# Performance work log

Hardware: AMD Instinct MI355X
Metric: run time of the kernel (lower is better)

Reference implementation:

```python
import jax, jax.numpy as jnp
import numpy as np

THRESH = 64.0        # titans.surprise_threshold
NOISE_SCALE = 1e-6   # tie-breaking noise scale in _update_memory


def setup_inputs() -> dict:
    key = jax.random.key(0)
    ks = jax.random.split(key, 8)
    B, S, H, M = 2, 2048, 1024, 8192
    return {
        "hidden_states": jax.random.normal(ks[0], (B, S, H), dtype=jnp.float32),
        "memory_buffer": jax.random.normal(ks[1], (M, H), dtype=jnp.float32),
        "importance_scores": jax.random.uniform(ks[2], (M,), dtype=jnp.float32),
        "Wq": jax.random.normal(ks[3], (H, H), dtype=jnp.float32) * 0.02,
        "bq": jnp.zeros((H,), dtype=jnp.float32),
        "Wk": jax.random.normal(ks[4], (H, H), dtype=jnp.float32) * 0.02,
        "bk": jnp.zeros((H,), dtype=jnp.float32),
        "noise": jax.random.normal(ks[5], (M,), dtype=jnp.float32),
    }


def reference(hidden_states, memory_buffer, importance_scores, Wq, bq, Wk, bk, noise):
    B, S, H = hidden_states.shape
    M = memory_buffer.shape[0]

    # ---- surprise (gradient_norm method) ----
    # proxy_loss = sum((h - 0)^2)  =>  d loss / d h = 2h  =>  surprise = 2*||h||_2
    cands = hidden_states.reshape(-1, H)                      # [B*S, H]
    surprise = 2.0 * jnp.linalg.norm(cands, axis=-1)          # [B*S]

    # ---- _update_memory (torch.no_grad) ----
    # mask below-threshold candidates out, then take the (at most memory_size)
    # most surprising candidates in descending order (== argsort descending +
    # slice in the torch code; -inf entries sort last and are marked invalid).
    K = min(cands.shape[0], M)
    masked = jnp.where(surprise > THRESH, surprise, -jnp.inf)
    top_s, top_i = jax.lax.top_k(masked, K)                   # descending surprise
    valid = top_s > THRESH                                    # true only for real candidates

    # least-important memory slots (topk largest=False with tie-break noise)
    _, least_idx = jax.lax.top_k(-(importance_scores + noise * NOISE_SCALE), K)

    # scatter-write: i-th most surprising candidate -> i-th least important slot.
    # invalid lanes write to index M which is dropped (out of range).
    write_idx = jnp.where(valid, least_idx, M)                # [K]
    states_w = jax.lax.stop_gradient(cands[top_i])            # update path is no_grad
    scores_w = jax.lax.stop_gradient(jnp.where(valid, top_s, 0.0))
    new_buffer = memory_buffer.at[write_idx].set(states_w, mode="drop")   # [M, H]
    new_importance = importance_scores.at[write_idx].set(scores_w, mode="drop")
    del new_importance  # bookkeeping state; does not affect retrieved output

    # ---- query (cross-attention over memory) ----
    q = hidden_states @ Wq.T + bq                             # [B, S, H]
    mk = new_buffer @ Wk.T + bk                               # [M, H]
    scores = jnp.einsum("bsh,mh->bsm", q, mk) * (H ** -0.5)
    attn = jax.nn.softmax(scores, axis=-1)                    # [B, S, M]
    retrieved = jnp.einsum("bsm,mh->bsh", attn, new_buffer)   # [B, S, H]
    return retrieved
```

## Files before the change

### kernel.cpp

```cpp
#include <hip/hip_runtime.h>
#include <hip/hip_bf16.h>
#include <math.h>
#include <stdint.h>

typedef __attribute__((ext_vector_type(4))) float floatx4;
typedef __attribute__((ext_vector_type(8))) short shortx8;
typedef __attribute__((ext_vector_type(8))) unsigned short ushortx8;
typedef __attribute__((ext_vector_type(4))) unsigned short ushortx4;

#define BS_CAND 4096
#define HDIM    1024
#define MSLOTS  8192
#define THRESH  64.0f
#define PV_SPLIT 4
#define PS_COLS 128

__device__ __forceinline__ unsigned short f2b_bits(float f) {
    __hip_bfloat16 b = __float2bfloat16(f);
    return *(unsigned short*)&b;
}
__device__ __forceinline__ float b2f_bits(unsigned short u) {
    return __uint_as_float(((unsigned)u) << 16);
}

__device__ __forceinline__ float blockReduceSum(float x) {
    __shared__ float red[4];
    #pragma unroll
    for (int o = 32; o > 0; o >>= 1) x += __shfl_down(x, o, 64);
    int lane = threadIdx.x & 63, w = threadIdx.x >> 6;
    if (lane == 0) red[w] = x;
    __syncthreads();
    float s = red[0] + red[1] + red[2] + red[3];
    __syncthreads();
    return s;
}

__global__ __launch_bounds__(256) void pre_k(const float* __restrict__ h,
                                             float* __restrict__ sur,
                                             __hip_bfloat16* __restrict__ Hbf,
                                             const float* __restrict__ imp,
                                             const float* __restrict__ noi,
                                             float* __restrict__ keys,
                                             int* __restrict__ row_src,
                                             const float* __restrict__ Wq,
                                             __hip_bfloat16* __restrict__ Wqbf,
                                             const float* __restrict__ Wk,
                                             __hip_bfloat16* __restrict__ Wkbf) {
    int b = blockIdx.x;
    if (b < BS_CAND) {
        float4 v = ((const float4*)(h + (size_t)b * HDIM))[threadIdx.x];
        ushortx4 o;
        o.x = f2b_bits(v.x); o.y = f2b_bits(v.y);
        o.z = f2b_bits(v.z); o.w = f2b_bits(v.w);
        ((ushortx4*)(Hbf + (size_t)b * HDIM))[threadIdx.x] = o;
        float s = v.x * v.x + v.y * v.y + v.z * v.z + v.w * v.w;
        float tot = blockReduceSum(s);
        if (threadIdx.x == 0) sur[b] = 2.0f * sqrtf(tot);
    } else if (b < BS_CAND + MSLOTS / 256) {
        int i = (b - BS_CAND) * 256 + threadIdx.x;
        keys[i] = imp[i] + noi[i] * 1e-6f;
        row_src[i] = -1;
    } else {
        int w = b - (BS_CAND + MSLOTS / 256);
        const float* in = (w < 1024) ? Wq : Wk;
        __hip_bfloat16* out = (w < 1024) ? Wqbf : Wkbf;
        int j = (w & 1023) * 256 + threadIdx.x;
        float4 v = ((const float4*)in)[j];
        ushortx4 o;
        o.x = f2b_bits(v.x); o.y = f2b_bits(v.y);
        o.z = f2b_bits(v.z); o.w = f2b_bits(v.w);
        ((ushortx4*)out)[j] = o;
    }
}

__global__ __launch_bounds__(256) void ranks_k(const float* __restrict__ sur,
                                               int* __restrict__ cand_ord,
                                               const float* __restrict__ keys,
                                               int* __restrict__ slot_ord) {
    int b = blockIdx.x;
    if (b < BS_CAND) {
        float ki = sur[b];
        float cnt = 0.f;
        for (int j = threadIdx.x; j < BS_CAND; j += 256) {
            float kj = sur[j];
            cnt += ((kj > ki) || (kj == ki && j < b)) ? 1.f : 0.f;
        }
        float r = blockReduceSum(cnt);
        if (threadIdx.x == 0) cand_ord[(int)r] = b;
    } else {
        int i = b - BS_CAND;
        float ki = keys[i];
        float cnt = 0.f;
        for (int j = threadIdx.x; j < MSLOTS; j += 256) {
            float kj = keys[j];
            cnt += ((kj < ki) || (kj == ki && j < i)) ? 1.f : 0.f;
        }
        float r = blockReduceSum(cnt);
        if (threadIdx.x == 0) slot_ord[(int)r] = i;
    }
}

__global__ __launch_bounds__(256) void scatter_k(const int* __restrict__ cand_order,
                                                 const int* __restrict__ slot_order,
                                                 const float* __restrict__ sur,
                                                 int* __restrict__ row_src) {
    int i = blockIdx.x * 256 + threadIdx.x;
    int c = cand_order[i];
    if (sur[c] > THRESH) row_src[slot_order[i]] = c;
}

__global__ __launch_bounds__(256) void build_b_k(const float* __restrict__ mem,
                                                 const float* __restrict__ hid,
                                                 const int* __restrict__ src,
                                                 __hip_bfloat16* __restrict__ B) {
    int m = blockIdx.x;
    int s = src[m];
    const float4* r = (const float4*)((s < 0) ? (mem + (size_t)m * HDIM)
                                              : (hid + (size_t)s * HDIM));
    float4 v = r[threadIdx.x];
    ushortx4 o;
    o.x = f2b_bits(v.x); o.y = f2b_bits(v.y);
    o.z = f2b_bits(v.z); o.w = f2b_bits(v.w);
    ((ushortx4*)(B + (size_t)m * HDIM))[threadIdx.x] = o;
}

__global__ __launch_bounds__(256) void transpose_k(const __hip_bfloat16* __restrict__ in,
                                                   __hip_bfloat16* __restrict__ out,
                                                   int R, int C) {
    __shared__ __hip_bfloat16 t[64][65];
    int cb = blockIdx.x * 64, rb = blockIdx.y * 64;
    int tx = threadIdx.x & 63, ty = threadIdx.x >> 6;
    #pragma unroll
    for (int k = 0; k < 16; k++) {
        int r = ty * 16 + k;
        t[r][tx] = in[(size_t)(rb + r) * C + cb + tx];
    }
    __syncthreads();
    #pragma unroll
    for (int k = 0; k < 16; k++) {
        int c = ty * 16 + k;
        out[(size_t)(cb + c) * R + rb + tx] = t[tx][c];
    }
}

__device__ __forceinline__ void load_lds16(const __hip_bfloat16* g, __hip_bfloat16* l) {
    __builtin_amdgcn_global_load_lds(
        (const __attribute__((address_space(1))) void*)g,
        (__attribute__((address_space(3))) void*)l, 16, 0, 0);
}

template <int EPI, int SWAP>
__global__ __launch_bounds__(256) void gemm_bt(const __hip_bfloat16* __restrict__ A,
                                               const __hip_bfloat16* __restrict__ Bt,
                                               const __hip_bfloat16* __restrict__ Bt2,
                                               __hip_bfloat16* __restrict__ outH,
                                               const float* __restrict__ bias,
                                               const float* __restrict__ bias2,
                                               float* __restrict__ ps,
                                               int rows0b,
                                               int M, int N, int K, int ksplit,
                                               float scale) {
    __shared__ alignas(16) __hip_bfloat16 Asm[2][128 * 32];
    __shared__ alignas(16) __hip_bfloat16 Bsm[2][128 * 32];
    const int tid = threadIdx.x;
    const int wave = tid >> 6, lane = tid & 63;
    const int bm = SWAP ? blockIdx.x : blockIdx.y;
    const int bn = SWAP ? blockIdx.y : blockIdx.x;
    const int kb = blockIdx.z * ksplit, ke = kb + ksplit;
    const int wr = (wave >> 1) * 64, wc = (wave & 1) * 64;
    const int lm = lane & 15, lq = lane >> 4;

    const __hip_bfloat16* BtSel = (EPI == 1 && bm >= rows0b) ? Bt2 : Bt;
    const float* biasSel = (EPI == 1 && bm >= rows0b) ? bias2 : bias;

    floatx4 acc[4][4];
    #pragma unroll
    for (int i = 0; i < 4; i++)
        #pragma unroll
        for (int j = 0; j < 4; j++) acc[i][j] = {0.f, 0.f, 0.f, 0.f};

    const __hip_bfloat16* Abase = A + (size_t)bm * 128 * K;
    const __hip_bfloat16* Bbase = BtSel + (size_t)bn * 128 * K;

    for (int k0 = kb; k0 < ke; k0 += 64) {
        #pragma unroll
        for (int t = 0; t < 4; t++) {
            int g = wave * 4 + t;
            int p = g >> 3;
            int pcb = (g & 7) << 6;
            int pc = pcb + lane;
            int row = pc >> 2, cc = pc & 3;
            load_lds16(Abase + (size_t)row * K + k0 + p * 32 + cc * 8,
                       &Asm[p][pcb * 8]);
        }
        #pragma unroll
        for (int t = 0; t < 4; t++) {
            int g = wave * 4 + t;
            int p = g >> 3;
            int pcb = (g & 7) << 6;
            int pc = pcb + lane;
            int row = pc >> 2, cc = pc & 3;
            load_lds16(Bbase + (size_t)row * K + k0 + p * 32 + cc * 8,
                       &Bsm[p][pcb * 8]);
        }
        __syncthreads();
        #pragma unroll
        for (int ks = 0; ks < 2; ks++) {
            shortx8 af[4], bfr[4];
            #pragma unroll
            for (int i = 0; i < 4; i++)
                af[i] = *(const shortx8*)(&Asm[ks][(wr + i * 16 + lm) * 32 + lq * 8]);
            #pragma unroll
            for (int j = 0; j < 4; j++)
                bfr[j] = *(const shortx8*)(&Bsm[ks][(wc + j * 16 + lm) * 32 + lq * 8]);
            #pragma unroll
            for (int i = 0; i < 4; i++)
                #pragma unroll
                for (int j = 0; j < 4; j++)
                    acc[i][j] = __builtin_amdgcn_mfma_f32_16x16x32_bf16(af[i], bfr[j],
                                                                        acc[i][j], 0, 0, 0);
        }
        __syncthreads();
    }

    if (EPI == 2) {
        #pragma unroll
        for (int i = 0; i < 4; i++) {
            int grow0 = bm * 128 + wr + i * 16 + lq * 4;
            #pragma unroll
            for (int r = 0; r < 4; r++) {
                float rs = 0.f;
                #pragma unroll
                for (int j = 0; j < 4; j++) {
                    int gcol = bn * 128 + wc + j * 16 + lm;
                    float e = __expf(acc[i][j][r] * scale);
                    unsigned short eb = f2b_bits(e);
                    ((unsigned short*)outH)[(size_t)(grow0 + r) * N + gcol] = eb;
                    rs += b2f_bits(eb);
                }
                rs += __shfl_xor(rs, 1, 64);
                rs += __shfl_xor(rs, 2, 64);
                rs += __shfl_xor(rs, 4, 64);
                rs += __shfl_xor(rs, 8, 64);
                if (lm == 0)
                    ps[(size_t)(grow0 + r) * PS_COLS + bn * 2 + (wave & 1)] = rs;
            }
        }
    } else {
        __hip_bfloat16* outHz = outH + ((EPI == 4) ? (size_t)blockIdx.z * M * N : 0);
        #pragma unroll
        for (int i = 0; i < 4; i++) {
            int grow0 = bm * 128 + wr + i * 16 + lq * 4;
            #pragma unroll
            for (int j = 0; j < 4; j++) {
                int gcol = bn * 128 + wc + j * 16 + lm;
                #pragma unroll
                for (int r = 0; r < 4; r++) {
                    float v = acc[i][j][r];
                    size_t idx = (size_t)(grow0 + r) * N + gcol;
                    if (EPI == 1) outHz[idx] = __float2bfloat16(v + biasSel[gcol]);
                    else          outHz[idx] = __float2bfloat16(v * scale);
                }
            }
        }
    }
}

__global__ __launch_bounds__(256) void reduce4_k(const ushortx4* __restrict__ part,
                                                 const float* __restrict__ ps,
                                                 float4* __restrict__ out) {
    int row = blockIdx.x;
    float s = 0.f;
    if (threadIdx.x < PS_COLS) s = ps[(size_t)row * PS_COLS + threadIdx.x];
    float tot = blockReduceSum(s);
    float inv = 1.f / tot;
    size_t base = (size_t)row * (HDIM / 4) + threadIdx.x;
    const size_t stride = (size_t)BS_CAND * (HDIM / 4);
    float4 o = {0.f, 0.f, 0.f, 0.f};
    #pragma unroll
    for (int z = 0; z < PV_SPLIT; z++) {
        ushortx4 p = part[base + (size_t)z * stride];
        o.x += b2f_bits(p.x); o.y += b2f_bits(p.y);
        o.z += b2f_bits(p.z); o.w += b2f_bits(p.w);
    }
    o.x *= inv; o.y *= inv; o.z *= inv; o.w *= inv;
    out[(size_t)row * (HDIM / 4) + threadIdx.x] = o;
}

extern "C" void kernel_launch(void* const* d_in, const int* in_sizes, int n_in,
                              void* d_out, int out_size, void* d_ws, size_t ws_size,
                              hipStream_t stream) {
    const float* hidden = (const float*)d_in[0];
    const float* membuf = (const float*)d_in[1];
    const float* imp    = (const float*)d_in[2];
    const float* Wq     = (const float*)d_in[3];
    const float* bq     = (const float*)d_in[4];
    const float* Wk     = (const float*)d_in[5];
    const float* bk     = (const float*)d_in[6];
    const float* noise  = (const float*)d_in[7];

    char* ws = (char*)d_ws;
    size_t off = 0;
    auto alloc = [&](size_t bytes) -> void* {
        void* p = ws + off;
        off += (bytes + 255) & ~(size_t)255;
        return p;
    };
    float*          surprise = (float*)alloc(BS_CAND * 4);
    float*          skeys    = (float*)alloc(MSLOTS * 4);
    float*          ps       = (float*)alloc((size_t)BS_CAND * PS_COLS * 4);
    int*            cand_ord = (int*)alloc(BS_CAND * 4);
    int*            slot_ord = (int*)alloc(MSLOTS * 4);
    int*            row_src  = (int*)alloc(MSLOTS * 4);
    __hip_bfloat16* Wqbf = (__hip_bfloat16*)alloc((size_t)HDIM * HDIM * 2);
    __hip_bfloat16* Wkbf = (__hip_bfloat16*)alloc((size_t)HDIM * HDIM * 2);
    __hip_bfloat16* BbfT = (__hip_bfloat16*)alloc((size_t)HDIM * MSLOTS * 2);
    size_t s_base = off;
    __hip_bfloat16* Sbf = (__hip_bfloat16*)(ws + s_base);
    __hip_bfloat16* Hbf = (__hip_bfloat16*)(ws + s_base);
    __hip_bfloat16* Bbf = (__hip_bfloat16*)(ws + s_base + (size_t)BS_CAND * HDIM * 2);
    off = s_base + ((size_t)BS_CAND * MSLOTS * 2 + 255) & ~(size_t)255;
    size_t t_base = off;
    __hip_bfloat16* qbf  = (__hip_bfloat16*)alloc((size_t)BS_CAND * HDIM * 2);
    __hip_bfloat16* mkbf = (__hip_bfloat16*)alloc((size_t)MSLOTS * HDIM * 2);
    __hip_bfloat16* part = (__hip_bfloat16*)(ws + t_base);

    pre_k<<<BS_CAND + MSLOTS / 256 + 2048, 256, 0, stream>>>(
        hidden, surprise, Hbf, imp, noise, skeys, row_src, Wq, Wqbf, Wk, Wkbf);
    ranks_k<<<BS_CAND + MSLOTS, 256, 0, stream>>>(surprise, cand_ord, skeys, slot_ord);
    scatter_k<<<BS_CAND / 256, 256, 0, stream>>>(cand_ord, slot_ord, surprise, row_src);
    build_b_k<<<MSLOTS, 256, 0, stream>>>(membuf, hidden, row_src, Bbf);
    transpose_k<<<dim3(HDIM / 64, MSLOTS / 64), 256, 0, stream>>>(Bbf, BbfT, MSLOTS, HDIM);
    gemm_bt<1, 0><<<dim3(HDIM / 128, (BS_CAND + MSLOTS) / 128), 256, 0, stream>>>(
        Hbf, Wqbf, Wkbf, qbf, bq, bk, nullptr, BS_CAND / 128,
        BS_CAND + MSLOTS, HDIM, HDIM, HDIM, 1.f);
    gemm_bt<2, 0><<<dim3(MSLOTS / 128, BS_CAND / 128), 256, 0, stream>>>(
        qbf, mkbf, nullptr, Sbf, nullptr, nullptr, ps, 1 << 30,
        BS_CAND, MSLOTS, HDIM, HDIM, 0.03125f);
    gemm_bt<4, 1><<<dim3(BS_CAND / 128, HDIM / 128, PV_SPLIT), 256, 0, stream>>>(
        Sbf, BbfT, nullptr, part, nullptr, nullptr, nullptr, 1 << 30,
        BS_CAND, HDIM, MSLOTS, MSLOTS / PV_SPLIT, 1.f);
    reduce4_k<<<BS_CAND, 256, 0, stream>>>((const ushortx4*)part, ps, (float4*)d_out);
}
```

Measured before the change: 364.1 us.

## Rewrite bf16 GEMM with 256x256 tiles, swizzled LDS and double-buffered pipeline

Replaces the 128x128, 4-wave GEMM with a 256x256 tile computed by 8 waves, each holding an 8x4 grid of MFMA accumulators. It stages 128-wide K slices into 128 KB of XOR-swizzled dynamic LDS with double buffering. Global-to-LDS loads are interleaved with MFMA quadrants using explicit barriers, vmcnt/lgkmcnt waits and s_setprio. The aim is more data reuse per LDS load, fewer bank conflicts and overlap of memory traffic with compute. In exchange, grids get smaller (the projection GEMM has only 192 blocks) and only one block fits per CU, so occupancy and the hand-written wait counts are a risk.

```diff
diff --git a/kernel.cpp b/kernel.cpp
--- a/kernel.cpp
+++ b/kernel.cpp
@@ -5,7 +5,6 @@
 
 typedef __attribute__((ext_vector_type(4))) float floatx4;
 typedef __attribute__((ext_vector_type(8))) short shortx8;
-typedef __attribute__((ext_vector_type(8))) unsigned short ushortx8;
 typedef __attribute__((ext_vector_type(4))) unsigned short ushortx4;
 
 #define BS_CAND 4096
@@ -150,89 +149,165 @@
 }
 
 template <int EPI, int SWAP>
-__global__ __launch_bounds__(256) void gemm_bt(const __hip_bfloat16* __restrict__ A,
-                                               const __hip_bfloat16* __restrict__ Bt,
-                                               const __hip_bfloat16* __restrict__ Bt2,
-                                               __hip_bfloat16* __restrict__ outH,
-                                               const float* __restrict__ bias,
-                                               const float* __restrict__ bias2,
-                                               float* __restrict__ ps,
-                                               int rows0b,
-                                               int M, int N, int K, int ksplit,
-                                               float scale) {
-    __shared__ alignas(16) __hip_bfloat16 Asm[2][128 * 32];
-    __shared__ alignas(16) __hip_bfloat16 Bsm[2][128 * 32];
+__global__ __launch_bounds__(512, 2) void gemm_bt(const __hip_bfloat16* __restrict__ A,
+                                                  const __hip_bfloat16* __restrict__ Bt,
+                                                  const __hip_bfloat16* __restrict__ Bt2,
+                                                  __hip_bfloat16* __restrict__ outH,
+                                                  const float* __restrict__ bias,
+                                                  const float* __restrict__ bias2,
+                                                  float* __restrict__ ps,
+                                                  int rows0b,
+                                                  int M, int N, int K, int ksplit,
+                                                  float scale) {
+    extern __shared__ char lds[];
     const int tid = threadIdx.x;
     const int wave = tid >> 6, lane = tid & 63;
+    const int lm = lane & 15, lq = lane >> 4;
+    const int wm = wave >> 2, wn = wave & 3;
     const int bm = SWAP ? blockIdx.x : blockIdx.y;
     const int bn = SWAP ? blockIdx.y : blockIdx.x;
-    const int kb = blockIdx.z * ksplit, ke = kb + ksplit;
-    const int wr = (wave >> 1) * 64, wc = (wave & 1) * 64;
-    const int lm = lane & 15, lq = lane >> 4;
+    const int kb = blockIdx.z * ksplit;
+    const int niters = ksplit >> 7;
 
     const __hip_bfloat16* BtSel = (EPI == 1 && bm >= rows0b) ? Bt2 : Bt;
     const float* biasSel = (EPI == 1 && bm >= rows0b) ? bias2 : bias;
 
-    floatx4 acc[4][4];
-    #pragma unroll
-    for (int i = 0; i < 4; i++)
+    const int l8 = lane >> 3;
+    const int colsrc = ((((lane & 7) << 4) ^ (l8 << 4)) >> 1);
+    const __hip_bfloat16* Abase = A + (size_t)bm * 256 * K;
+    const __hip_bfloat16* Bbase = BtSel + (size_t)bn * 256 * K;
+    const __hip_bfloat16* srcA[2][2];
+    const __hip_bfloat16* srcB[2][2];
+    #pragma unroll
+    for (int h = 0; h < 2; h++)
+        #pragma unroll
+        for (int t = 0; t < 2; t++) {
+            int row = t * 128 + h * 64 + wave * 8 + l8;
+            srcA[h][t] = Abase + (size_t)row * K + colsrc;
+            srcB[h][t] = Bbase + (size_t)row * K + colsrc;
+        }
+
+    const int cxor = (lq << 4) ^ ((lm & 7) << 4);
+    const int a_b0 = (wm * 64 + lm) * 128 + cxor;
+    const int a_b1 = a_b0 ^ 64;
+    const int b_b0 = (wn * 32 + lm) * 128 + cxor;
+    const int b_b1 = b_b0 ^ 64;
+
+    floatx4 acc[8][4];
+    #pragma unroll
+    for (int i = 0; i < 8; i++)
         #pragma unroll
         for (int j = 0; j < 4; j++) acc[i][j] = {0.f, 0.f, 0.f, 0.f};
 
-    const __hip_bfloat16* Abase = A + (size_t)bm * 128 * K;
-    const __hip_bfloat16* Bbase = BtSel + (size_t)bn * 128 * K;
-
-    for (int k0 = kb; k0 < ke; k0 += 64) {
-        #pragma unroll
-        for (int t = 0; t < 4; t++) {
-            int g = wave * 4 + t;
-            int p = g >> 3;
-            int pcb = (g & 7) << 6;
-            int pc = pcb + lane;
-            int row = pc >> 2, cc = pc & 3;
-            load_lds16(Abase + (size_t)row * K + k0 + p * 32 + cc * 8,
-                       &Asm[p][pcb * 8]);
-        }
-        #pragma unroll
-        for (int t = 0; t < 4; t++) {
-            int g = wave * 4 + t;
-            int p = g >> 3;
-            int pcb = (g & 7) << 6;
-            int pc = pcb + lane;
-            int row = pc >> 2, cc = pc & 3;
-            load_lds16(Bbase + (size_t)row * K + k0 + p * 32 + cc * 8,
-                       &Bsm[p][pcb * 8]);
-        }
-        __syncthreads();
-        #pragma unroll
-        for (int ks = 0; ks < 2; ks++) {
-            shortx8 af[4], bfr[4];
-            #pragma unroll
-            for (int i = 0; i < 4; i++)
-                af[i] = *(const shortx8*)(&Asm[ks][(wr + i * 16 + lm) * 32 + lq * 8]);
-            #pragma unroll
-            for (int j = 0; j < 4; j++)
-                bfr[j] = *(const shortx8*)(&Bsm[ks][(wc + j * 16 + lm) * 32 + lq * 8]);
-            #pragma unroll
-            for (int i = 0; i < 4; i++)
-                #pragma unroll
-                for (int j = 0; j < 4; j++)
-                    acc[i][j] = __builtin_amdgcn_mfma_f32_16x16x32_bf16(af[i], bfr[j],
-                                                                        acc[i][j], 0, 0, 0);
-        }
-        __syncthreads();
-    }
+    shortx8 af[4][2], bf[2][2];
+
+#define LDSV(off) (*(const shortx8*)(lds + (off)))
+#define READ_A(g, bo) do {                                                  \
+    const int ab_ = (bo) + (g) * 16384;                                     \
+    af[0][0] = LDSV(ab_ + a_b0);        af[0][1] = LDSV(ab_ + a_b1);        \
+    af[1][0] = LDSV(ab_ + a_b0 + 2048); af[1][1] = LDSV(ab_ + a_b1 + 2048); \
+    af[2][0] = LDSV(ab_ + a_b0 + 4096); af[2][1] = LDSV(ab_ + a_b1 + 4096); \
+    af[3][0] = LDSV(ab_ + a_b0 + 6144); af[3][1] = LDSV(ab_ + a_b1 + 6144); \
+} while (0)
+#define READ_B(g, bo) do {                                                  \
+    const int bb_ = (bo) + 32768 + (g) * 16384;                             \
+    bf[0][0] = LDSV(bb_ + b_b0);        bf[0][1] = LDSV(bb_ + b_b1);        \
+    bf[1][0] = LDSV(bb_ + b_b0 + 2048); bf[1][1] = LDSV(bb_ + b_b1 + 2048); \
+} while (0)
+#define STAGE(xs, h, buf, kofs) do {                                        \
+    char* d_ = lds + (buf) * 65536 + (xs) * 32768 + (h) * 16384 + wave * 1024; \
+    load_lds16(((xs) ? srcB : srcA)[h][0] + (kofs), (__hip_bfloat16*)d_);   \
+    load_lds16(((xs) ? srcB : srcA)[h][1] + (kofs), (__hip_bfloat16*)(d_ + 8192)); \
+} while (0)
+#define MFQ(mh, nh) do {                                                    \
+    __builtin_amdgcn_s_setprio(1);                                          \
+    _Pragma("unroll")                                                       \
+    for (int ii_ = 0; ii_ < 4; ii_++)                                       \
+        _Pragma("unroll")                                                   \
+        for (int jj_ = 0; jj_ < 2; jj_++) {                                 \
+            acc[(mh)*4+ii_][(nh)*2+jj_] = __builtin_amdgcn_mfma_f32_16x16x32_bf16( \
+                af[ii_][0], bf[jj_][0], acc[(mh)*4+ii_][(nh)*2+jj_], 0, 0, 0); \
+            acc[(mh)*4+ii_][(nh)*2+jj_] = __builtin_amdgcn_mfma_f32_16x16x32_bf16( \
+                af[ii_][1], bf[jj_][1], acc[(mh)*4+ii_][(nh)*2+jj_], 0, 0, 0); \
+        }                                                                   \
+    __builtin_amdgcn_s_setprio(0);                                          \
+} while (0)
+#define BAR() __builtin_amdgcn_s_barrier()
+#define LGKM0() asm volatile("s_waitcnt lgkmcnt(0)" ::: "memory")
+#define VMC6() asm volatile("s_waitcnt vmcnt(6)" ::: "memory")
+#define VMC0() asm volatile("s_waitcnt vmcnt(0)" ::: "memory")
+
+    STAGE(0, 0, 0, kb);
+    STAGE(1, 1, 0, kb);
+    STAGE(0, 1, 0, kb);
+    STAGE(1, 0, 0, kb);
+    STAGE(0, 0, 1, kb + 64);
+    STAGE(1, 1, 1, kb + 64);
+    STAGE(0, 1, 1, kb + 64);
+    VMC6();
+    BAR();
+
+#define ITER(E, kcur, knext) do {                                           \
+                                         \
+    READ_A(0, 0); READ_B(0, 0); STAGE(1, 0, 1, (kcur) + 64);                \
+    BAR(); LGKM0(); MFQ(0, 0); BAR();                                       \
+                                                                   \
+    READ_B(1, 0); if (E) STAGE(0, 0, 0, (knext));                           \
+    BAR(); LGKM0(); MFQ(0, 1); BAR();                                       \
+                                                                   \
+    READ_A(1, 0); if (E) STAGE(1, 1, 0, (knext));                           \
+    BAR(); LGKM0(); MFQ(1, 1); BAR();                                       \
+                                                                   \
+    READ_B(0, 0);                                                           \
+    if (E) { STAGE(0, 1, 0, (knext)); VMC6(); } else { VMC0(); }            \
+    BAR(); LGKM0(); MFQ(1, 0); BAR();                                       \
+                                         \
+    READ_A(0, 65536); READ_B(0, 65536); if (E) STAGE(1, 0, 0, (knext));     \
+    BAR(); LGKM0(); MFQ(0, 0); BAR();                                       \
+                                                                   \
+    READ_B(1, 65536); if (E) STAGE(0, 0, 1, (knext) + 64);                  \
+    BAR(); LGKM0(); MFQ(0, 1); BAR();                                       \
+                                                                   \
+    READ_A(1, 65536); if (E) STAGE(1, 1, 1, (knext) + 64);                  \
+    BAR(); LGKM0(); MFQ(1, 1); BAR();                                       \
+                                                                   \
+    READ_B(0, 65536); if (E) { STAGE(0, 1, 1, (knext) + 64); VMC6(); }      \
+    BAR(); LGKM0(); MFQ(1, 0); BAR();                                       \
+} while (0)
+
+    int it = 0;
+    #pragma unroll 1
+    for (; it < niters - 1; ++it) {
+        const int kc = kb + it * 128;
+        ITER(1, kc, kc + 128);
+    }
+    {
+        const int kc = kb + it * 128;
+        ITER(0, kc, 0);
+    }
+
+#undef ITER
+#undef LDSV
+#undef READ_A
+#undef READ_B
+#undef STAGE
+#undef MFQ
+#undef BAR
+#undef LGKM0
+#undef VMC6
+#undef VMC0
 
     if (EPI == 2) {
         #pragma unroll
-        for (int i = 0; i < 4; i++) {
-            int grow0 = bm * 128 + wr + i * 16 + lq * 4;
+        for (int i = 0; i < 8; i++) {
+            const int grow0 = bm * 256 + wm * 128 + (i >> 2) * 64 + (i & 3) * 16 + lq * 4;
             #pragma unroll
             for (int r = 0; r < 4; r++) {
                 float rs = 0.f;
                 #pragma unroll
                 for (int j = 0; j < 4; j++) {
-                    int gcol = bn * 128 + wc + j * 16 + lm;
+                    const int gcol = bn * 256 + (wn >> 1) * 128 + (j >> 1) * 64 +
+                                     (wn & 1) * 32 + (j & 1) * 16 + lm;
                     float e = __expf(acc[i][j][r] * scale);
                     unsigned short eb = f2b_bits(e);
                     ((unsigned short*)outH)[(size_t)(grow0 + r) * N + gcol] = eb;
@@ -243,17 +318,18 @@
                 rs += __shfl_xor(rs, 4, 64);
                 rs += __shfl_xor(rs, 8, 64);
                 if (lm == 0)
-                    ps[(size_t)(grow0 + r) * PS_COLS + bn * 2 + (wave & 1)] = rs;
+                    ps[(size_t)(grow0 + r) * PS_COLS + bn * 4 + wn] = rs;
             }
         }
     } else {
         __hip_bfloat16* outHz = outH + ((EPI == 4) ? (size_t)blockIdx.z * M * N : 0);
         #pragma unroll
-        for (int i = 0; i < 4; i++) {
-            int grow0 = bm * 128 + wr + i * 16 + lq * 4;
+        for (int i = 0; i < 8; i++) {
+            const int grow0 = bm * 256 + wm * 128 + (i >> 2) * 64 + (i & 3) * 16 + lq * 4;
             #pragma unroll
             for (int j = 0; j < 4; j++) {
-                int gcol = bn * 128 + wc + j * 16 + lm;
+                const int gcol = bn * 256 + (wn >> 1) * 128 + (j >> 1) * 64 +
+                                 (wn & 1) * 32 + (j & 1) * 16 + lm;
                 #pragma unroll
                 for (int r = 0; r < 4; r++) {
                     float v = acc[i][j][r];
@@ -298,6 +374,17 @@
     const float* Wk     = (const float*)d_in[5];
     const float* bk     = (const float*)d_in[6];
     const float* noise  = (const float*)d_in[7];
+
+    static bool s_attr = false;
+    if (!s_attr) {
+        (void)hipFuncSetAttribute((const void*)gemm_bt<1, 0>,
+                                  hipFuncAttributeMaxDynamicSharedMemorySize, 131072);
+        (void)hipFuncSetAttribute((const void*)gemm_bt<2, 0>,
+                                  hipFuncAttributeMaxDynamicSharedMemorySize, 131072);
+        (void)hipFuncSetAttribute((const void*)gemm_bt<4, 1>,
+                                  hipFuncAttributeMaxDynamicSharedMemorySize, 131072);
+        s_attr = true;
+    }
 
     char* ws = (char*)d_ws;
     size_t off = 0;
@@ -331,13 +418,13 @@
     scatter_k<<<BS_CAND / 256, 256, 0, stream>>>(cand_ord, slot_ord, surprise, row_src);
     build_b_k<<<MSLOTS, 256, 0, stream>>>(membuf, hidden, row_src, Bbf);
     transpose_k<<<dim3(HDIM / 64, MSLOTS / 64), 256, 0, stream>>>(Bbf, BbfT, MSLOTS, HDIM);
-    gemm_bt<1, 0><<<dim3(HDIM / 128, (BS_CAND + MSLOTS) / 128), 256, 0, stream>>>(
-        Hbf, Wqbf, Wkbf, qbf, bq, bk, nullptr, BS_CAND / 128,
+    gemm_bt<1, 0><<<dim3(HDIM / 256, (BS_CAND + MSLOTS) / 256), 512, 131072, stream>>>(
+        Hbf, Wqbf, Wkbf, qbf, bq, bk, nullptr, BS_CAND / 256,
         BS_CAND + MSLOTS, HDIM, HDIM, HDIM, 1.f);
-    gemm_bt<2, 0><<<dim3(MSLOTS / 128, BS_CAND / 128), 256, 0, stream>>>(
+    gemm_bt<2, 0><<<dim3(MSLOTS / 256, BS_CAND / 256), 512, 131072, stream>>>(
         qbf, mkbf, nullptr, Sbf, nullptr, nullptr, ps, 1 << 30,
         BS_CAND, MSLOTS, HDIM, HDIM, 0.03125f);
-    gemm_bt<4, 1><<<dim3(BS_CAND / 128, HDIM / 128, PV_SPLIT), 256, 0, stream>>>(
+    gemm_bt<4, 1><<<dim3(BS_CAND / 256, HDIM / 256, PV_SPLIT), 512, 131072, stream>>>(
         Sbf, BbfT, nullptr, part, nullptr, nullptr, nullptr, 1 << 30,
         BS_CAND, HDIM, MSLOTS, MSLOTS / PV_SPLIT, 1.f);
     reduce4_k<<<BS_CAND, 256, 0, stream>>>((const ushortx4*)part, ps, (float4*)d_out);
```

New measurement: 316.0 us. 1.15x faster.
